# Kernel tuning notes

Measured on AMD Instinct MI355X. Metric: run time of the kernel, lower is better.

## Reference

```python
import jax, jax.numpy as jnp
import numpy as np

NODE_DIM = 64
DEPTH = 2
N = 50000          # node_size
DEG = 24           # average degree
E = N * DEG        # triple_size = 1.2M edges
R = 500            # rel_size
FEAT = NODE_DIM * (DEPTH + 1)  # 192


def _l2norm(x, eps=1e-12):
    # torch F.normalize(p=2): x / max(||x||, eps)
    n = jnp.sqrt(jnp.sum(x * x, axis=-1, keepdims=True))
    return x / jnp.maximum(n, eps)


def setup_inputs() -> dict:
    key = jax.random.key(0)
    ks = jax.random.split(key, 8)
    features = jax.random.normal(ks[0], (N, NODE_DIM), jnp.float32)
    rel_emb = jax.random.normal(ks[1], (R, NODE_DIM), jnp.float32)
    # duplicate-free edge list, rows sorted (matches a coalesced sparse adj)
    rows = jnp.repeat(jnp.arange(N, dtype=jnp.int32), DEG)
    offs = jnp.tile(1 + jnp.arange(DEG, dtype=jnp.int32) * 7, N)
    cols = (rows + offs) % N
    adj = jnp.stack([rows, cols])  # [2, E]
    # sparse [E, R] triple->relation matrix: one relation per triple
    r_index = jnp.stack([jnp.arange(E, dtype=jnp.int32),
                         jax.random.randint(ks[2], (E,), 0, R, jnp.int32)])
    r_val = jax.random.uniform(ks[3], (E,), jnp.float32, 0.5, 1.5)
    # params (xavier-ish scales)
    proxy = jax.random.normal(ks[4], (64, FEAT), jnp.float32) * (1.0 / np.sqrt(FEAT))
    gate_w = jax.random.normal(ks[5], (FEAT, FEAT), jnp.float32) * (1.0 / np.sqrt(FEAT))
    gate_b = jnp.zeros((FEAT,), jnp.float32)
    attn_kernels = jax.random.normal(ks[6], (DEPTH, NODE_DIM), jnp.float32) * 0.1
    return {"features": features, "rel_emb": rel_emb, "proxy": proxy,
            "gate_w": gate_w, "gate_b": gate_b, "attn_kernels": attn_kernels,
            "adj": adj, "r_index": r_index, "r_val": r_val,
            "triple_size": E, "rel_size": R, "node_size": N}


def reference(features, rel_emb, proxy, gate_w, gate_b, attn_kernels,
              adj, r_index, r_val, triple_size, rel_size, node_size):
    feats = jnp.tanh(features)
    outs = [feats]
    dst = adj[0]  # rows: softmax / scatter-sum segment ids
    src = adj[1]  # cols: neighbor gather ids
    for l in range(attn_kernels.shape[0]):
        neighs = feats[src]                                  # [E, d] gather
        # sparse.mm(tri_rel, rel_emb): sum_k r_val * rel_emb[rel_id] per triple
        tri_rel = jax.ops.segment_sum(r_val[:, None] * rel_emb[r_index[1]],
                                      r_index[0], num_segments=triple_size)
        tri_rel = _l2norm(tri_rel)                           # [E, d]
        # relational reflection: h - 2 <h, r> r
        neighs = neighs - 2.0 * jnp.sum(neighs * tri_rel, axis=1, keepdims=True) * tri_rel
        att = jnp.einsum('ed,d->e', tri_rel, attn_kernels[l])  # [E]
        # sparse softmax over rows of adjacency (segment softmax over dst)
        m = jax.ops.segment_max(att, dst, num_segments=node_size)
        ex = jnp.exp(att - m[dst])
        denom = jax.ops.segment_sum(ex, dst, num_segments=node_size)
        w = ex / denom[dst]
        new_f = jax.ops.segment_sum(neighs * w[:, None], dst, num_segments=node_size)
        feats = jnp.tanh(new_f)
        outs.append(feats)
    outputs = jnp.concatenate(outs, axis=-1)                 # [N, feat]
    proxy_att = jax.nn.softmax(_l2norm(outputs) @ _l2norm(proxy).T, axis=-1)
    proxy_feature = outputs - proxy_att @ proxy
    gate = jax.nn.sigmoid(proxy_feature @ gate_w.T + gate_b)
    return gate * outputs + (1.0 - gate) * proxy_feature
```

## Files before the change

### kernel.cpp

```cpp
#include <hip/hip_runtime.h>
#include <hip/hip_bf16.h>
#include <cstdint>
#include <cstddef>

#define N_NODES 50000
#define DEG     24
#define NEDGE   (N_NODES*DEG)
#define RSZ     500
#define NDIM    64
#define FEATD   192

#define LSTR    200

#define LGRID   1568
#define LCHUNK  196

typedef short bf16x8 __attribute__((ext_vector_type(8)));
typedef float f32x4  __attribute__((ext_vector_type(4)));

__device__ __forceinline__ unsigned short f2bf(float f) {
    unsigned u = __builtin_bit_cast(unsigned, f);
    unsigned r = (u + 0x7fffu + ((u >> 16) & 1u)) >> 16;
    return (unsigned short)r;
}
__device__ __forceinline__ float bf2f(unsigned short s) {
    unsigned u = ((unsigned)s) << 16;
    return __builtin_bit_cast(float, u);
}
__device__ __forceinline__ float fast_tanh(float x) {
    float e = __expf(2.f * x);
    return 1.f - 2.f / (e + 1.f);
}

__global__ __launch_bounds__(256) void k_prep(const float* __restrict__ features,
                                              const float* __restrict__ rel_emb,
                                              const float* __restrict__ attn_k,
                                              const float* __restrict__ proxy,
                                              const float* __restrict__ gate_w,
                                              const int* __restrict__ src,
                                              const int* __restrict__ rel,
                                              float* __restrict__ fin0,
                                              float* __restrict__ reln,
                                              float* __restrict__ expdot,
                                              float* __restrict__ pninv,
                                              unsigned short* __restrict__ B1,
                                              unsigned short* __restrict__ B2,
                                              unsigned short* __restrict__ B3,
                                              unsigned int* __restrict__ pedge) {
    int b = blockIdx.x;
    if (b < 3125) {
        int t = b * 256 + threadIdx.x;
        int idx4 = t * 4;
        float4 f = *reinterpret_cast<const float4*>(features + idx4);
        float4 o;
        o.x = fast_tanh(f.x); o.y = fast_tanh(f.y);
        o.z = fast_tanh(f.z); o.w = fast_tanh(f.w);
        *reinterpret_cast<float4*>(fin0 + idx4) = o;
    } else if (b < 3250) {
        int lane = threadIdx.x & 63;
        int row = (b - 3125) * 4 + (threadIdx.x >> 6);
        float v = rel_emb[row * 64 + lane];
        float ss = v * v;
        for (int m = 1; m < 64; m <<= 1) ss += __shfl_xor(ss, m);
        float inv = 1.f / fmaxf(sqrtf(ss), 1e-12f);
        float rn = v * inv;
        reln[row * 64 + lane] = rn;
        float d0 = rn * attn_k[lane];
        float d1 = rn * attn_k[64 + lane];
        for (int m = 1; m < 64; m <<= 1) { d0 += __shfl_xor(d0, m); d1 += __shfl_xor(d1, m); }
        if (lane == 0) { expdot[row] = __expf(d0); expdot[RSZ + row] = __expf(d1); }
    } else if (b < 3266) {
        int lane = threadIdx.x & 63;
        int row = (b - 3250) * 4 + (threadIdx.x >> 6);
        const float* p = proxy + (size_t)row * FEATD;
        float a = p[lane], bb = p[64 + lane], c = p[128 + lane];
        float ss = a * a + bb * bb + c * c;
        for (int m = 1; m < 64; m <<= 1) ss += __shfl_xor(ss, m);
        if (lane == 0) pninv[row] = 1.f / fmaxf(sqrtf(ss), 1e-12f);
    } else if (b < 3506) {
        int idx = (b - 3266) * 256 + threadIdx.x;
        int j = idx & 7, lane = (idx >> 3) & 63;
        int t = idx >> 9;
        int lane16 = lane & 15, quad = lane >> 4;
        if (t < 24) {
            int kt = t >> 2, nt = t & 3;
            int k = kt * 32 + quad * 8 + j, n = nt * 16 + lane16;
            B1[idx] = f2bf(proxy[(size_t)n * FEATD + k]);
        } else if (t < 48) {
            int tt = t - 24, kt = tt / 12, nt = tt % 12;
            int k = kt * 32 + quad * 8 + j, n = nt * 16 + lane16;
            B2[idx - 12288] = f2bf(proxy[(size_t)k * FEATD + n]);
        } else {
            int tt = t - 48, kt = tt / 12, nt = tt % 12;
            int k = kt * 32 + quad * 8 + j, n = nt * 16 + lane16;
            B3[idx - 24576] = f2bf(gate_w[(size_t)n * FEATD + k]);
        }
    } else {
        int t = (b - 3506) * 256 + threadIdx.x;
        if (t < NEDGE / 4) {
            int4 s4 = *reinterpret_cast<const int4*>(src + t * 4);
            int4 r4 = *reinterpret_cast<const int4*>(rel + t * 4);
            uint4 o;
            o.x = (unsigned)s4.x | ((unsigned)r4.x << 16);
            o.y = (unsigned)s4.y | ((unsigned)r4.y << 16);
            o.z = (unsigned)s4.z | ((unsigned)r4.z << 16);
            o.w = (unsigned)s4.w | ((unsigned)r4.w << 16);
            *reinterpret_cast<uint4*>(pedge + t * 4) = o;
        }
    }
}

__global__ __launch_bounds__(256) void k_layer(const unsigned int* __restrict__ pedge,
                                               const float* __restrict__ reln,
                                               const float* __restrict__ expdot_l,
                                               const float* __restrict__ fin,
                                               float* __restrict__ fout) {
    int b = blockIdx.x;
    int lb = (b & 7) * LCHUNK + (b >> 3);
    int lane8 = threadIdx.x & 7;
    int node = lb * 32 + (threadIdx.x >> 3);
    if (node >= N_NODES) return;
    int ebase = node * DEG;
    unsigned pk[DEG];
#pragma unroll
    for (int k = 0; k < DEG; k++) pk[k] = pedge[ebase + k];
    float a0 = 0.f, a1 = 0.f, a2 = 0.f, a3 = 0.f;
    float a4 = 0.f, a5 = 0.f, a6 = 0.f, a7 = 0.f, den = 0.f;
#pragma unroll 4
    for (int k = 0; k < DEG; k++) {
        unsigned p = pk[k];
        int s = p & 0xFFFF;
        int r = p >> 16;
        float ex = expdot_l[r];
        const float* tp = reln + (size_t)r * 64 + lane8 * 8;
        const float* np = fin + (size_t)s * 64 + lane8 * 8;
        float4 t0 = *reinterpret_cast<const float4*>(tp);
        float4 t1v = *reinterpret_cast<const float4*>(tp + 4);
        float4 n0 = *reinterpret_cast<const float4*>(np);
        float4 n1v = *reinterpret_cast<const float4*>(np + 4);
        float pd = t0.x * n0.x + t0.y * n0.y + t0.z * n0.z + t0.w * n0.w
                 + t1v.x * n1v.x + t1v.y * n1v.y + t1v.z * n1v.z + t1v.w * n1v.w;
        pd += __shfl_xor(pd, 1); pd += __shfl_xor(pd, 2); pd += __shfl_xor(pd, 4);
        float t1 = -2.f * pd * ex;
        a0 = fmaf(ex, n0.x, fmaf(t1, t0.x, a0));
        a1 = fmaf(ex, n0.y, fmaf(t1, t0.y, a1));
        a2 = fmaf(ex, n0.z, fmaf(t1, t0.z, a2));
        a3 = fmaf(ex, n0.w, fmaf(t1, t0.w, a3));
        a4 = fmaf(ex, n1v.x, fmaf(t1, t1v.x, a4));
        a5 = fmaf(ex, n1v.y, fmaf(t1, t1v.y, a5));
        a6 = fmaf(ex, n1v.z, fmaf(t1, t1v.z, a6));
        a7 = fmaf(ex, n1v.w, fmaf(t1, t1v.w, a7));
        den += ex;
    }
    float id = 1.f / den;
    float4 o0, o1;
    o0.x = fast_tanh(a0 * id); o0.y = fast_tanh(a1 * id);
    o0.z = fast_tanh(a2 * id); o0.w = fast_tanh(a3 * id);
    o1.x = fast_tanh(a4 * id); o1.y = fast_tanh(a5 * id);
    o1.z = fast_tanh(a6 * id); o1.w = fast_tanh(a7 * id);
    float* f = fout + (size_t)node * 64 + lane8 * 8;
    *reinterpret_cast<float4*>(f) = o0;
    *reinterpret_cast<float4*>(f + 4) = o1;
}

__global__ __launch_bounds__(256) void k_gate(const float* __restrict__ fin0,
                                              const float* __restrict__ fin1,
                                              const float* __restrict__ fin2,
                                              const unsigned short* __restrict__ B1,
                                              const unsigned short* __restrict__ B2,
                                              const unsigned short* __restrict__ B3,
                                              const float* __restrict__ pninv,
                                              const float* __restrict__ gate_b,
                                              float* __restrict__ dout) {
    __shared__ unsigned short lds[4][16 * LSTR];
    int wv = threadIdx.x >> 6, lane = threadIdx.x & 63;
    int tile = blockIdx.x * 4 + wv;
    if (tile > N_NODES / 16 - 1) tile = N_NODES / 16 - 1;
    int row0 = tile * 16, lane16 = lane & 15, quad = lane >> 4;
    unsigned short* L = lds[wv];
    const float* fsel[3] = {fin0, fin1, fin2};

    float oreg[12][4];
#pragma unroll
    for (int nt = 0; nt < 12; nt++) {
        const float* f = fsel[nt >> 2];
#pragma unroll
        for (int r = 0; r < 4; r++)
            oreg[nt][r] = f[(size_t)(row0 + quad * 4 + r) * 64 + (nt & 3) * 16 + lane16];
    }

    bf16x8 af[6];
    float ss = 0.f;
#pragma unroll
    for (int kt = 0; kt < 6; kt++) {
        const float* f = fsel[kt >> 1];
        const float* arow = f + (size_t)(row0 + lane16) * 64 + (kt & 1) * 32 + quad * 8;
        float4 p0 = *reinterpret_cast<const float4*>(arow);
        float4 p1 = *reinterpret_cast<const float4*>(arow + 4);
        ss += p0.x * p0.x + p0.y * p0.y + p0.z * p0.z + p0.w * p0.w;
        ss += p1.x * p1.x + p1.y * p1.y + p1.z * p1.z + p1.w * p1.w;
        bf16x8 a;
        a[0] = (short)f2bf(p0.x); a[1] = (short)f2bf(p0.y);
        a[2] = (short)f2bf(p0.z); a[3] = (short)f2bf(p0.w);
        a[4] = (short)f2bf(p1.x); a[5] = (short)f2bf(p1.y);
        a[6] = (short)f2bf(p1.z); a[7] = (short)f2bf(p1.w);
        af[kt] = a;
    }
    ss += __shfl_xor(ss, 16); ss += __shfl_xor(ss, 32);
    float inv = 1.f / fmaxf(sqrtf(ss), 1e-12f);
    float pni[4];
#pragma unroll
    for (int nt = 0; nt < 4; nt++) pni[nt] = pninv[nt * 16 + lane16];
    f32x4 acc4[4];
#pragma unroll
    for (int nt = 0; nt < 4; nt++) acc4[nt] = (f32x4){0.f, 0.f, 0.f, 0.f};
#pragma unroll
    for (int kt = 0; kt < 6; kt++) {
#pragma unroll
        for (int nt = 0; nt < 4; nt++) {
            bf16x8 bfr = *reinterpret_cast<const bf16x8*>(B1 + ((size_t)(kt * 4 + nt) * 64 + lane) * 8);
            acc4[nt] = __builtin_amdgcn_mfma_f32_16x16x32_bf16(af[kt], bfr, acc4[nt], 0, 0, 0);
        }
    }
#pragma unroll
    for (int r = 0; r < 4; r++) {
        int rowloc = quad * 4 + r;
        float invr = __shfl(inv, rowloc);
        float e0 = __expf(acc4[0][r] * invr * pni[0]);
        float e1 = __expf(acc4[1][r] * invr * pni[1]);
        float e2 = __expf(acc4[2][r] * invr * pni[2]);
        float e3 = __expf(acc4[3][r] * invr * pni[3]);
        float s = e0 + e1 + e2 + e3;
        s += __shfl_xor(s, 1); s += __shfl_xor(s, 2);
        s += __shfl_xor(s, 4); s += __shfl_xor(s, 8);
        float rs = 1.f / s;
        L[rowloc * LSTR + lane16]      = f2bf(e0 * rs);
        L[rowloc * LSTR + 16 + lane16] = f2bf(e1 * rs);
        L[rowloc * LSTR + 32 + lane16] = f2bf(e2 * rs);
        L[rowloc * LSTR + 48 + lane16] = f2bf(e3 * rs);
    }
    __threadfence_block();

    f32x4 acc[12];
#pragma unroll
    for (int nt = 0; nt < 12; nt++) acc[nt] = (f32x4){0.f, 0.f, 0.f, 0.f};
#pragma unroll
    for (int kt = 0; kt < 2; kt++) {
        bf16x8 a = *reinterpret_cast<const bf16x8*>(L + lane16 * LSTR + kt * 32 + quad * 8);
#pragma unroll
        for (int nt = 0; nt < 12; nt++) {
            bf16x8 bfr = *reinterpret_cast<const bf16x8*>(B2 + ((size_t)(kt * 12 + nt) * 64 + lane) * 8);
            acc[nt] = __builtin_amdgcn_mfma_f32_16x16x32_bf16(a, bfr, acc[nt], 0, 0, 0);
        }
    }
    __threadfence_block();
#pragma unroll
    for (int nt = 0; nt < 12; nt++) {
#pragma unroll
        for (int r = 0; r < 4; r++) {
            int rowloc = quad * 4 + r;
            L[rowloc * LSTR + nt * 16 + lane16] = f2bf(oreg[nt][r] - acc[nt][r]);
        }
    }
    __threadfence_block();

#pragma unroll
    for (int nt = 0; nt < 12; nt++) acc[nt] = (f32x4){0.f, 0.f, 0.f, 0.f};
#pragma unroll
    for (int kt = 0; kt < 6; kt++) {
        bf16x8 a = *reinterpret_cast<const bf16x8*>(L + lane16 * LSTR + kt * 32 + quad * 8);
#pragma unroll
        for (int nt = 0; nt < 12; nt++) {
            bf16x8 bfr = *reinterpret_cast<const bf16x8*>(B3 + ((size_t)(kt * 12 + nt) * 64 + lane) * 8);
            acc[nt] = __builtin_amdgcn_mfma_f32_16x16x32_bf16(a, bfr, acc[nt], 0, 0, 0);
        }
    }

#pragma unroll
    for (int nt = 0; nt < 12; nt++) {
        float bias = gate_b[nt * 16 + lane16];
#pragma unroll
        for (int r = 0; r < 4; r++) {
            int rowloc = quad * 4 + r;
            size_t idx = (size_t)(row0 + rowloc) * FEATD + nt * 16 + lane16;
            float z = acc[nt][r] + bias;
            float g = 1.f / (1.f + __expf(-z));
            float pf = bf2f(L[rowloc * LSTR + nt * 16 + lane16]);
            dout[idx] = pf + g * (oreg[nt][r] - pf);
        }
    }
}

extern "C" void kernel_launch(void* const* d_in, const int* in_sizes, int n_in,
                              void* d_out, int out_size, void* d_ws, size_t ws_size,
                              hipStream_t stream) {
    (void)in_sizes; (void)n_in; (void)out_size; (void)ws_size;
    const float* features = (const float*)d_in[0];
    const float* rel_emb  = (const float*)d_in[1];
    const float* proxy    = (const float*)d_in[2];
    const float* gate_w   = (const float*)d_in[3];
    const float* gate_b   = (const float*)d_in[4];
    const float* attn_k   = (const float*)d_in[5];
    const int*   adj      = (const int*)d_in[6];
    const int*   r_index  = (const int*)d_in[7];

    float* fin0    = (float*)d_ws;
    float* fin1    = fin0 + (size_t)N_NODES * 64;
    float* fin2    = fin1 + (size_t)N_NODES * 64;
    float* reln    = fin2 + (size_t)N_NODES * 64;
    float* expdot  = reln + RSZ * 64;
    float* pninv   = expdot + 2 * RSZ;
    unsigned short* B1 = (unsigned short*)(pninv + 64);
    unsigned short* B2 = B1 + 12288;
    unsigned short* B3 = B2 + 12288;
    unsigned int* pedge = (unsigned int*)(B3 + 36864);

    const int* src = adj + NEDGE;
    const int* rel = r_index + NEDGE;

    k_prep  <<<dim3(4678), dim3(256), 0, stream>>>(features, rel_emb, attn_k, proxy, gate_w,
                                                   src, rel, fin0, reln, expdot,
                                                   pninv, B1, B2, B3, pedge);
    k_layer <<<dim3(LGRID), dim3(256), 0, stream>>>(pedge, reln, expdot,       fin0, fin1);
    k_layer <<<dim3(LGRID), dim3(256), 0, stream>>>(pedge, reln, expdot + RSZ, fin1, fin2);
    k_gate  <<<dim3(782),  dim3(256), 0, stream>>>(fin0, fin1, fin2, B1, B2, B3, pninv,
                                                   gate_b, (float*)d_out);
}
```

Before: 205.3 us.

## Precompute proxy·gate_w product so gate GEMMs run off outputs and attention directly

```diff
diff --git a/kernel.cpp b/kernel.cpp
--- a/kernel.cpp
+++ b/kernel.cpp
@@ -10,7 +10,7 @@
 #define NDIM    64
 #define FEATD   192
 
-#define LSTR    200
+#define PASTR   72
 
 #define LGRID   1568
 #define LCHUNK  196
@@ -22,10 +22,6 @@
     unsigned u = __builtin_bit_cast(unsigned, f);
     unsigned r = (u + 0x7fffu + ((u >> 16) & 1u)) >> 16;
     return (unsigned short)r;
-}
-__device__ __forceinline__ float bf2f(unsigned short s) {
-    unsigned u = ((unsigned)s) << 16;
-    return __builtin_bit_cast(float, u);
 }
 __device__ __forceinline__ float fast_tanh(float x) {
     float e = __expf(2.f * x);
@@ -46,6 +42,7 @@
                                               unsigned short* __restrict__ B1,
                                               unsigned short* __restrict__ B2,
                                               unsigned short* __restrict__ B3,
+                                              unsigned short* __restrict__ B4,
                                               unsigned int* __restrict__ pedge) {
     int b = blockIdx.x;
     if (b < 3125) {
@@ -95,7 +92,7 @@
             int k = kt * 32 + quad * 8 + j, n = nt * 16 + lane16;
             B3[idx - 24576] = f2bf(gate_w[(size_t)n * FEATD + k]);
         }
-    } else {
+    } else if (b < 4678) {
         int t = (b - 3506) * 256 + threadIdx.x;
         if (t < NEDGE / 4) {
             int4 s4 = *reinterpret_cast<const int4*>(src + t * 4);
@@ -107,6 +104,21 @@
             o.w = (unsigned)s4.w | ((unsigned)r4.w << 16);
             *reinterpret_cast<uint4*>(pedge + t * 4) = o;
         }
+    } else {
+        int t = (b - 4678) * 256 + threadIdx.x;
+        int j = t & 7, lane = (t >> 3) & 63, tl = t >> 9;
+        int lane16 = lane & 15, quad = lane >> 4;
+        int kt = tl / 12, nt = tl % 12;
+        int k = kt * 32 + quad * 8 + j, n = nt * 16 + lane16;
+        const float4* pr = reinterpret_cast<const float4*>(proxy + (size_t)k * FEATD);
+        const float4* gr = reinterpret_cast<const float4*>(gate_w + (size_t)n * FEATD);
+        float acc = 0.f;
+#pragma unroll 8
+        for (int q = 0; q < 48; q++) {
+            float4 a = pr[q], g4 = gr[q];
+            acc += a.x * g4.x + a.y * g4.y + a.z * g4.z + a.w * g4.w;
+        }
+        B4[t] = f2bf(acc);
     }
 }
 
@@ -163,31 +175,23 @@
     *reinterpret_cast<float4*>(f + 4) = o1;
 }
 
-__global__ __launch_bounds__(256) void k_gate(const float* __restrict__ fin0,
-                                              const float* __restrict__ fin1,
-                                              const float* __restrict__ fin2,
-                                              const unsigned short* __restrict__ B1,
-                                              const unsigned short* __restrict__ B2,
-                                              const unsigned short* __restrict__ B3,
-                                              const float* __restrict__ pninv,
-                                              const float* __restrict__ gate_b,
-                                              float* __restrict__ dout) {
-    __shared__ unsigned short lds[4][16 * LSTR];
+__global__ __launch_bounds__(256, 3) void k_gate(const float* __restrict__ fin0,
+                                                 const float* __restrict__ fin1,
+                                                 const float* __restrict__ fin2,
+                                                 const unsigned short* __restrict__ B1,
+                                                 const unsigned short* __restrict__ B2,
+                                                 const unsigned short* __restrict__ B3,
+                                                 const unsigned short* __restrict__ B4,
+                                                 const float* __restrict__ pninv,
+                                                 const float* __restrict__ gate_b,
+                                                 float* __restrict__ dout) {
+    __shared__ unsigned short lds[4][16 * PASTR];
     int wv = threadIdx.x >> 6, lane = threadIdx.x & 63;
     int tile = blockIdx.x * 4 + wv;
     if (tile > N_NODES / 16 - 1) tile = N_NODES / 16 - 1;
     int row0 = tile * 16, lane16 = lane & 15, quad = lane >> 4;
     unsigned short* L = lds[wv];
     const float* fsel[3] = {fin0, fin1, fin2};
-
-    float oreg[12][4];
-#pragma unroll
-    for (int nt = 0; nt < 12; nt++) {
-        const float* f = fsel[nt >> 2];
-#pragma unroll
-        for (int r = 0; r < 4; r++)
-            oreg[nt][r] = f[(size_t)(row0 + quad * 4 + r) * 64 + (nt & 3) * 16 + lane16];
-    }
 
     bf16x8 af[6];
     float ss = 0.f;
@@ -211,6 +215,7 @@
     float pni[4];
 #pragma unroll
     for (int nt = 0; nt < 4; nt++) pni[nt] = pninv[nt * 16 + lane16];
+
     f32x4 acc4[4];
 #pragma unroll
     for (int nt = 0; nt < 4; nt++) acc4[nt] = (f32x4){0.f, 0.f, 0.f, 0.f};
@@ -234,59 +239,58 @@
         s += __shfl_xor(s, 1); s += __shfl_xor(s, 2);
         s += __shfl_xor(s, 4); s += __shfl_xor(s, 8);
         float rs = 1.f / s;
-        L[rowloc * LSTR + lane16]      = f2bf(e0 * rs);
-        L[rowloc * LSTR + 16 + lane16] = f2bf(e1 * rs);
-        L[rowloc * LSTR + 32 + lane16] = f2bf(e2 * rs);
-        L[rowloc * LSTR + 48 + lane16] = f2bf(e3 * rs);
+        L[rowloc * PASTR + lane16]      = f2bf(e0 * rs);
+        L[rowloc * PASTR + 16 + lane16] = f2bf(e1 * rs);
+        L[rowloc * PASTR + 32 + lane16] = f2bf(e2 * rs);
+        L[rowloc * PASTR + 48 + lane16] = f2bf(e3 * rs);
     }
     __threadfence_block();
 
-    f32x4 acc[12];
-#pragma unroll
-    for (int nt = 0; nt < 12; nt++) acc[nt] = (f32x4){0.f, 0.f, 0.f, 0.f};
-#pragma unroll
-    for (int kt = 0; kt < 2; kt++) {
-        bf16x8 a = *reinterpret_cast<const bf16x8*>(L + lane16 * LSTR + kt * 32 + quad * 8);
-#pragma unroll
-        for (int nt = 0; nt < 12; nt++) {
-            bf16x8 bfr = *reinterpret_cast<const bf16x8*>(B2 + ((size_t)(kt * 12 + nt) * 64 + lane) * 8);
-            acc[nt] = __builtin_amdgcn_mfma_f32_16x16x32_bf16(a, bfr, acc[nt], 0, 0, 0);
-        }
-    }
-    __threadfence_block();
-#pragma unroll
-    for (int nt = 0; nt < 12; nt++) {
-#pragma unroll
-        for (int r = 0; r < 4; r++) {
-            int rowloc = quad * 4 + r;
-            L[rowloc * LSTR + nt * 16 + lane16] = f2bf(oreg[nt][r] - acc[nt][r]);
-        }
-    }
-    __threadfence_block();
-
-#pragma unroll
-    for (int nt = 0; nt < 12; nt++) acc[nt] = (f32x4){0.f, 0.f, 0.f, 0.f};
-#pragma unroll
-    for (int kt = 0; kt < 6; kt++) {
-        bf16x8 a = *reinterpret_cast<const bf16x8*>(L + lane16 * LSTR + kt * 32 + quad * 8);
-#pragma unroll
-        for (int nt = 0; nt < 12; nt++) {
-            bf16x8 bfr = *reinterpret_cast<const bf16x8*>(B3 + ((size_t)(kt * 12 + nt) * 64 + lane) * 8);
-            acc[nt] = __builtin_amdgcn_mfma_f32_16x16x32_bf16(a, bfr, acc[nt], 0, 0, 0);
-        }
-    }
-
-#pragma unroll
-    for (int nt = 0; nt < 12; nt++) {
-        float bias = gate_b[nt * 16 + lane16];
-#pragma unroll
-        for (int r = 0; r < 4; r++) {
-            int rowloc = quad * 4 + r;
-            size_t idx = (size_t)(row0 + rowloc) * FEATD + nt * 16 + lane16;
-            float z = acc[nt][r] + bias;
-            float g = 1.f / (1.f + __expf(-z));
-            float pf = bf2f(L[rowloc * LSTR + nt * 16 + lane16]);
-            dout[idx] = pf + g * (oreg[nt][r] - pf);
+    bf16x8 paf[2];
+    paf[0] = *reinterpret_cast<const bf16x8*>(L + lane16 * PASTR + quad * 8);
+    paf[1] = *reinterpret_cast<const bf16x8*>(L + lane16 * PASTR + 32 + quad * 8);
+
+#pragma unroll
+    for (int h = 0; h < 2; h++) {
+        int nt0 = h * 6;
+        f32x4 s3[6], s4[6], s2[6];
+#pragma unroll
+        for (int n = 0; n < 6; n++) {
+            s3[n] = (f32x4){0.f, 0.f, 0.f, 0.f};
+            s4[n] = (f32x4){0.f, 0.f, 0.f, 0.f};
+            s2[n] = (f32x4){0.f, 0.f, 0.f, 0.f};
+        }
+#pragma unroll
+        for (int kt = 0; kt < 6; kt++) {
+#pragma unroll
+            for (int n = 0; n < 6; n++) {
+                bf16x8 bfr = *reinterpret_cast<const bf16x8*>(B3 + ((size_t)(kt * 12 + nt0 + n) * 64 + lane) * 8);
+                s3[n] = __builtin_amdgcn_mfma_f32_16x16x32_bf16(af[kt], bfr, s3[n], 0, 0, 0);
+            }
+        }
+#pragma unroll
+        for (int kt = 0; kt < 2; kt++) {
+#pragma unroll
+            for (int n = 0; n < 6; n++) {
+                bf16x8 b4 = *reinterpret_cast<const bf16x8*>(B4 + ((size_t)(kt * 12 + nt0 + n) * 64 + lane) * 8);
+                s4[n] = __builtin_amdgcn_mfma_f32_16x16x32_bf16(paf[kt], b4, s4[n], 0, 0, 0);
+                bf16x8 b2 = *reinterpret_cast<const bf16x8*>(B2 + ((size_t)(kt * 12 + nt0 + n) * 64 + lane) * 8);
+                s2[n] = __builtin_amdgcn_mfma_f32_16x16x32_bf16(paf[kt], b2, s2[n], 0, 0, 0);
+            }
+        }
+#pragma unroll
+        for (int n = 0; n < 6; n++) {
+            int nt = nt0 + n;
+            float bias = gate_b[nt * 16 + lane16];
+            const float* f = fsel[nt >> 2];
+#pragma unroll
+            for (int r = 0; r < 4; r++) {
+                int rowloc = quad * 4 + r;
+                float o = f[(size_t)(row0 + rowloc) * 64 + (nt & 3) * 16 + lane16];
+                float z = s3[n][r] - s4[n][r] + bias;
+                float g = 1.f / (1.f + __expf(-z));
+                dout[(size_t)(row0 + rowloc) * FEATD + nt * 16 + lane16] = o - (1.f - g) * s2[n][r];
+            }
         }
     }
 }
@@ -313,16 +317,17 @@
     unsigned short* B1 = (unsigned short*)(pninv + 64);
     unsigned short* B2 = B1 + 12288;
     unsigned short* B3 = B2 + 12288;
-    unsigned int* pedge = (unsigned int*)(B3 + 36864);
+    unsigned short* B4 = B3 + 36864;
+    unsigned int* pedge = (unsigned int*)(B4 + 12288);
 
     const int* src = adj + NEDGE;
     const int* rel = r_index + NEDGE;
 
-    k_prep  <<<dim3(4678), dim3(256), 0, stream>>>(features, rel_emb, attn_k, proxy, gate_w,
+    k_prep  <<<dim3(4726), dim3(256), 0, stream>>>(features, rel_emb, attn_k, proxy, gate_w,
                                                    src, rel, fin0, reln, expdot,
-                                                   pninv, B1, B2, B3, pedge);
+                                                   pninv, B1, B2, B3, B4, pedge);
     k_layer <<<dim3(LGRID), dim3(256), 0, stream>>>(pedge, reln, expdot,       fin0, fin1);
     k_layer <<<dim3(LGRID), dim3(256), 0, stream>>>(pedge, reln, expdot + RSZ, fin1, fin2);
-    k_gate  <<<dim3(782),  dim3(256), 0, stream>>>(fin0, fin1, fin2, B1, B2, B3, pninv,
+    k_gate  <<<dim3(782),  dim3(256), 0, stream>>>(fin0, fin1, fin2, B1, B2, B3, B4, pninv,
                                                    gate_b, (float*)d_out);
 }
```

Result: slower. 225.5 us (+9.8%).

## Stage neighbor feature window in LDS for layer aggregation

Applied to the files above, without the earlier changes.

```diff
diff --git a/kernel.cpp b/kernel.cpp
--- a/kernel.cpp
+++ b/kernel.cpp
@@ -12,8 +12,11 @@
 
 #define LSTR    200
 
-#define LGRID   1568
-#define LCHUNK  196
+#define WNODES  64
+#define WROWS   225
+#define WSTR    72
+#define LGRID   784
+#define LCHUNK  98
 
 typedef short bf16x8 __attribute__((ext_vector_type(8)));
 typedef float f32x4  __attribute__((ext_vector_type(4)));
@@ -115,52 +118,58 @@
                                                const float* __restrict__ expdot_l,
                                                const float* __restrict__ fin,
                                                float* __restrict__ fout) {
+    __shared__ float W[WROWS * WSTR];
     int b = blockIdx.x;
     int lb = (b & 7) * LCHUNK + (b >> 3);
-    int lane8 = threadIdx.x & 7;
-    int node = lb * 32 + (threadIdx.x >> 3);
-    if (node >= N_NODES) return;
-    int ebase = node * DEG;
-    unsigned pk[DEG];
-#pragma unroll
-    for (int k = 0; k < DEG; k++) pk[k] = pedge[ebase + k];
-    float a0 = 0.f, a1 = 0.f, a2 = 0.f, a3 = 0.f;
-    float a4 = 0.f, a5 = 0.f, a6 = 0.f, a7 = 0.f, den = 0.f;
-#pragma unroll 4
-    for (int k = 0; k < DEG; k++) {
-        unsigned p = pk[k];
-        int s = p & 0xFFFF;
-        int r = p >> 16;
-        float ex = expdot_l[r];
-        const float* tp = reln + (size_t)r * 64 + lane8 * 8;
-        const float* np = fin + (size_t)s * 64 + lane8 * 8;
-        float4 t0 = *reinterpret_cast<const float4*>(tp);
-        float4 t1v = *reinterpret_cast<const float4*>(tp + 4);
-        float4 n0 = *reinterpret_cast<const float4*>(np);
-        float4 n1v = *reinterpret_cast<const float4*>(np + 4);
-        float pd = t0.x * n0.x + t0.y * n0.y + t0.z * n0.z + t0.w * n0.w
-                 + t1v.x * n1v.x + t1v.y * n1v.y + t1v.z * n1v.z + t1v.w * n1v.w;
-        pd += __shfl_xor(pd, 1); pd += __shfl_xor(pd, 2); pd += __shfl_xor(pd, 4);
-        float t1 = -2.f * pd * ex;
-        a0 = fmaf(ex, n0.x, fmaf(t1, t0.x, a0));
-        a1 = fmaf(ex, n0.y, fmaf(t1, t0.y, a1));
-        a2 = fmaf(ex, n0.z, fmaf(t1, t0.z, a2));
-        a3 = fmaf(ex, n0.w, fmaf(t1, t0.w, a3));
-        a4 = fmaf(ex, n1v.x, fmaf(t1, t1v.x, a4));
-        a5 = fmaf(ex, n1v.y, fmaf(t1, t1v.y, a5));
-        a6 = fmaf(ex, n1v.z, fmaf(t1, t1v.z, a6));
-        a7 = fmaf(ex, n1v.w, fmaf(t1, t1v.w, a7));
-        den += ex;
-    }
-    float id = 1.f / den;
-    float4 o0, o1;
-    o0.x = fast_tanh(a0 * id); o0.y = fast_tanh(a1 * id);
-    o0.z = fast_tanh(a2 * id); o0.w = fast_tanh(a3 * id);
-    o1.x = fast_tanh(a4 * id); o1.y = fast_tanh(a5 * id);
-    o1.z = fast_tanh(a6 * id); o1.w = fast_tanh(a7 * id);
-    float* f = fout + (size_t)node * 64 + lane8 * 8;
-    *reinterpret_cast<float4*>(f) = o0;
-    *reinterpret_cast<float4*>(f + 4) = o1;
+    int B0 = lb * WNODES;
+    if (B0 >= N_NODES) return;
+
+    for (int i = threadIdx.x; i < WROWS * 16; i += 256) {
+        int row = i >> 4, c4 = (i & 15) * 4;
+        int g = B0 + 1 + row; if (g >= N_NODES) g -= N_NODES;
+        float4 v = *reinterpret_cast<const float4*>(fin + (size_t)g * 64 + c4);
+        *reinterpret_cast<float4*>(W + row * WSTR + c4) = v;
+    }
+    __syncthreads();
+
+    int lane16 = threadIdx.x & 15;
+    int wv = threadIdx.x >> 6;
+    int sub = (threadIdx.x >> 4) & 3;
+
+#pragma unroll
+    for (int g = 0; g < 4; g++) {
+        int node = B0 + ((g << 2) | wv) * 4 + sub;
+        bool valid = node < N_NODES;
+        int ebase = valid ? node * DEG : 0;
+        float a0 = 0.f, a1 = 0.f, a2 = 0.f, a3 = 0.f, den = 0.f;
+#pragma unroll 8
+        for (int k = 0; k < DEG; k++) {
+            unsigned pe = pedge[ebase + k];
+            int s = pe & 0xFFFF, r = pe >> 16;
+            float ex = expdot_l[r];
+            float4 tv = *reinterpret_cast<const float4*>(reln + (size_t)r * 64 + lane16 * 4);
+            int li = s - B0 - 1; if (li < 0) li += N_NODES;
+            float4 nv;
+            if (li < WROWS) nv = *reinterpret_cast<const float4*>(W + li * WSTR + lane16 * 4);
+            else            nv = *reinterpret_cast<const float4*>(fin + (size_t)s * 64 + lane16 * 4);
+            float pd = tv.x * nv.x + tv.y * nv.y + tv.z * nv.z + tv.w * nv.w;
+            pd += __shfl_xor(pd, 1); pd += __shfl_xor(pd, 2);
+            pd += __shfl_xor(pd, 4); pd += __shfl_xor(pd, 8);
+            float t1 = -2.f * pd * ex;
+            a0 = fmaf(ex, nv.x, fmaf(t1, tv.x, a0));
+            a1 = fmaf(ex, nv.y, fmaf(t1, tv.y, a1));
+            a2 = fmaf(ex, nv.z, fmaf(t1, tv.z, a2));
+            a3 = fmaf(ex, nv.w, fmaf(t1, tv.w, a3));
+            den += ex;
+        }
+        if (valid) {
+            float id = 1.f / den;
+            float4 o;
+            o.x = fast_tanh(a0 * id); o.y = fast_tanh(a1 * id);
+            o.z = fast_tanh(a2 * id); o.w = fast_tanh(a3 * id);
+            *reinterpret_cast<float4*>(fout + (size_t)node * 64 + lane16 * 4) = o;
+        }
+    }
 }
 
 __global__ __launch_bounds__(256) void k_gate(const float* __restrict__ fin0,
```

Measured after the change: 279.7 us. 1.36x slower.
